# Optimization experiments

Measured on AMD Instinct MI355X. Metric: run time of the kernel, lower is better.

The kernel has to match this reference:

```python
import jax, jax.numpy as jnp
import numpy as np

TEMPERATURE = 0.07
NEG = -9e15  # matches torch masked_fill value
EPS = 1e-8   # torch.nn.functional.cosine_similarity eps


def setup_inputs() -> dict:
    key = jax.random.key(0)
    k1, k2 = jax.random.split(key)
    B, D = 4096, 512
    return {
        "feats1": jax.random.normal(k1, (B, D), dtype=jnp.float32),
        "feats2": jax.random.normal(k2, (B, D), dtype=jnp.float32),
    }


def reference(feats1, feats2):
    feats = jnp.concatenate([feats1, feats2], axis=0)            # [2N, D]
    n = feats.shape[0]
    # cosine similarity via normalize-once + GEMM (same math as the
    # broadcasted F.cosine_similarity, incl. per-vector eps clamp)
    norms = jnp.maximum(jnp.linalg.norm(feats, axis=-1, keepdims=True), EPS)
    fn = feats / norms                                            # [2N, D]
    cos_sim = fn @ fn.T                                           # [2N, 2N]
    # mask self-similarity BEFORE temperature division (as in torch code)
    idx = jnp.arange(n)
    cos_sim = jnp.where(idx[:, None] == idx[None, :], NEG, cos_sim)
    cos_sim = cos_sim / TEMPERATURE
    # positive pair: eye rolled by N rows -> column (i + N) mod 2N
    pos_idx = (idx + n // 2) % n
    pos = cos_sim[idx, pos_idx]                                   # [2N]
    nll = jnp.mean(-pos + jax.nn.logsumexp(cos_sim, axis=-1))
    # ranking: rank of the positive among [pos, masked negatives];
    # equals # of masked entries strictly greater than pos
    masked = jnp.where(idx[None, :] == pos_idx[:, None], NEG, cos_sim)
    rank = jnp.sum(masked > pos[:, None], axis=-1)                # int [2N]
    acc_top1 = jnp.mean((rank == 0).astype(jnp.float32))
    acc_top5 = jnp.mean((rank < 5).astype(jnp.float32))
    acc_mean_pos = 1.0 + jnp.mean(rank.astype(jnp.float32))
    return (nll, acc_top1, acc_top5, acc_mean_pos)
```

## Files before the change

kernel.cpp:

```cpp
#include <hip/hip_runtime.h>
#include <math.h>
#include <stdint.h>

#define NTOT   8192
#define HALF_N 4096
#define DIM    512
#define INV_T  14.2857142857142857f
#define NTILE  64
#define NBLK   2080

using s16x8 = __attribute__((ext_vector_type(8))) short;
using f32x4 = __attribute__((ext_vector_type(4))) float;

__device__ unsigned short g_fnb[NTOT * DIM];
__device__ float g_pos[NTOT];
__device__ float g_ps[NTILE * NTOT];
__device__ int   g_pc[NTILE * NTOT];
__device__ float g_sumexp[NTOT];
__device__ int   g_cnt[NTOT];

__device__ __forceinline__ float bf2f(unsigned short u) {
  union { unsigned int i; float f; } v; v.i = ((unsigned int)u) << 16; return v.f;
}
__device__ __forceinline__ unsigned short f2bf(float x) {
  union { float f; unsigned int i; } v; v.f = x;
  unsigned int u = v.i;
  return (unsigned short)((u + 0x7FFFu + ((u >> 16) & 1u)) >> 16);
}

__device__ __forceinline__ void gload16(const unsigned short* g, unsigned short* l) {
  __builtin_amdgcn_global_load_lds(
      (const __attribute__((address_space(1))) unsigned int*)g,
      (__attribute__((address_space(3))) unsigned int*)l, 16, 0, 0);
}

__global__ __launch_bounds__(256) void knorm(const float* __restrict__ f1,
                                             const float* __restrict__ f2) {
  const int tid  = threadIdx.x;
  const int wv   = tid >> 6;
  const int pi   = wv >> 1;
  const int half = wv & 1;
  const int lane = tid & 63;
  const int b    = blockIdx.x * 2 + pi;
  const int row  = b + half * HALF_N;

  const float* src = (half == 0) ? (f1 + (size_t)b * DIM) : (f2 + (size_t)b * DIM);
  float4 v0 = ((const float4*)src)[lane];
  float4 v1 = ((const float4*)src)[lane + 64];
  float ss = v0.x*v0.x + v0.y*v0.y + v0.z*v0.z + v0.w*v0.w
           + v1.x*v1.x + v1.y*v1.y + v1.z*v1.z + v1.w*v1.w;
  #pragma unroll
  for (int o = 32; o >= 1; o >>= 1) ss += __shfl_xor(ss, o, 64);
  const float sc = 1.0f / fmaxf(sqrtf(ss), 1e-8f);
  ushort4 h0, h1;
  h0.x = f2bf(v0.x * sc); h0.y = f2bf(v0.y * sc);
  h0.z = f2bf(v0.z * sc); h0.w = f2bf(v0.w * sc);
  h1.x = f2bf(v1.x * sc); h1.y = f2bf(v1.y * sc);
  h1.z = f2bf(v1.z * sc); h1.w = f2bf(v1.w * sc);
  ushort4* dst = (ushort4*)(g_fnb + (size_t)row * DIM);
  dst[lane]      = h0;
  dst[lane + 64] = h1;

  __shared__ ushort4 sh[2][64][2];
  if (half == 1) { sh[pi][lane][0] = h0; sh[pi][lane][1] = h1; }
  __syncthreads();
  if (half == 0) {
    const ushort4 p0 = sh[pi][lane][0], p1 = sh[pi][lane][1];
    float s = bf2f(h0.x)*bf2f(p0.x) + bf2f(h0.y)*bf2f(p0.y)
            + bf2f(h0.z)*bf2f(p0.z) + bf2f(h0.w)*bf2f(p0.w)
            + bf2f(h1.x)*bf2f(p1.x) + bf2f(h1.y)*bf2f(p1.y)
            + bf2f(h1.z)*bf2f(p1.z) + bf2f(h1.w)*bf2f(p1.w);
    #pragma unroll
    for (int o = 32; o >= 1; o >>= 1) s += __shfl_xor(s, o, 64);
    if (lane == 0) { g_pos[b] = s; g_pos[b + HALF_N] = s; }
  }
}

__global__ __launch_bounds__(256, 4) void kmain() {
  __shared__ __align__(16) unsigned short As[128 * 64];
  __shared__ __align__(16) unsigned short Bs[128 * 64];
  __shared__ float sRowS[128]; __shared__ int sRowC[128];
  __shared__ float sColS[128]; __shared__ int sColC[128];

  int t = (blockIdx.x & 7) * (NBLK / 8) + (blockIdx.x >> 3);
  int bi = 0, rem = NTILE;
  while (t >= rem) { t -= rem; --rem; ++bi; }
  const int bj = bi + t;
  const bool offdiag = (bi != bj);
  const int i0 = bi * 128, j0 = bj * 128;

  const int tid  = threadIdx.x;
  const int lane = tid & 63;
  const int w    = tid >> 6;
  const int wr   = (w >> 1) * 64;
  const int wc   = (w & 1) * 64;
  const int lrow = lane & 15;
  const int lq   = lane >> 4;

  const int rsub = lane >> 3;
  const int lcb  = (lane & 7) ^ rsub;
  const unsigned short* Ag = g_fnb + (size_t)(i0 + w * 32 + rsub) * DIM + lcb * 8;
  const unsigned short* Bg = g_fnb + (size_t)(j0 + w * 32 + rsub) * DIM + lcb * 8;
  unsigned short* Al = &As[w * 32 * 64];
  unsigned short* Bl = &Bs[w * 32 * 64];

  f32x4 acc[4][4];
  #pragma unroll
  for (int a = 0; a < 4; ++a)
    #pragma unroll
    for (int bb = 0; bb < 4; ++bb) { acc[a][bb][0]=0.f; acc[a][bb][1]=0.f; acc[a][bb][2]=0.f; acc[a][bb][3]=0.f; }

  const unsigned short* Bls = offdiag ? (const unsigned short*)Bs
                                      : (const unsigned short*)As;

  for (int kt = 0; kt < 8; ++kt) {
    __syncthreads();
    const int kb = kt * 64;
    #pragma unroll
    for (int q = 0; q < 4; ++q) {
      gload16(Ag + (size_t)(q * 8) * DIM + kb, Al + q * 512);
      if (offdiag) gload16(Bg + (size_t)(q * 8) * DIM + kb, Bl + q * 512);
    }
    __syncthreads();

    #pragma unroll
    for (int kk = 0; kk < 2; ++kk) {
      s16x8 af[4], bf[4];
      #pragma unroll
      for (int mi = 0; mi < 4; ++mi) {
        const int r = wr + mi * 16 + lrow;
        af[mi] = *(const s16x8*)(&As[r * 64 + (((kk * 4 + lq) ^ (lrow & 7)) * 8)]);
      }
      #pragma unroll
      for (int ni = 0; ni < 4; ++ni) {
        const int r = wc + ni * 16 + lrow;
        bf[ni] = *(const s16x8*)(&Bls[r * 64 + (((kk * 4 + lq) ^ (lrow & 7)) * 8)]);
      }
      #pragma unroll
      for (int mi = 0; mi < 4; ++mi)
        #pragma unroll
        for (int ni = 0; ni < 4; ++ni)
          acc[mi][ni] = __builtin_amdgcn_mfma_f32_16x16x32_bf16(af[mi], bf[ni], acc[mi][ni], 0, 0, 0);
    }
  }

  if (tid < 128) { sRowS[tid] = 0.f; sRowC[tid] = 0; sColS[tid] = 0.f; sColC[tid] = 0; }
  __syncthreads();

  #pragma unroll
  for (int mi = 0; mi < 4; ++mi) {
    #pragma unroll
    for (int r = 0; r < 4; ++r) {
      const int ridx = wr + mi * 16 + lq * 4 + r;
      const int i  = i0 + ridx;
      const float pv = g_pos[i];
      float s = 0.f; int c = 0;
      #pragma unroll
      for (int ni = 0; ni < 4; ++ni) {
        const int j = j0 + wc + ni * 16 + lrow;
        const float v = acc[mi][ni][r];
        const float e = __expf(v * INV_T);
        const bool diag = (j == i);
        s += diag ? 0.f : e;
        c += (!diag && (j != (i ^ HALF_N)) && (v > pv)) ? 1 : 0;
      }
      #pragma unroll
      for (int o = 1; o < 16; o <<= 1) {
        s += __shfl_xor(s, o, 64);
        c += __shfl_xor(c, o, 64);
      }
      if (lrow == 0) {
        atomicAdd(&sRowS[ridx], s);
        atomicAdd(&sRowC[ridx], c);
      }
    }
  }

  if (offdiag) {
    #pragma unroll
    for (int ni = 0; ni < 4; ++ni) {
      const int cidx = wc + ni * 16 + lrow;
      const int j  = j0 + cidx;
      const float pj = g_pos[j];
      float s = 0.f; int c = 0;
      #pragma unroll
      for (int mi = 0; mi < 4; ++mi) {
        #pragma unroll
        for (int r = 0; r < 4; ++r) {
          const int i = i0 + wr + mi * 16 + lq * 4 + r;
          const float v = acc[mi][ni][r];
          s += __expf(v * INV_T);
          c += ((i != (j ^ HALF_N)) && (v > pj)) ? 1 : 0;
        }
      }
      s += __shfl_xor(s, 16, 64); s += __shfl_xor(s, 32, 64);
      c += __shfl_xor(c, 16, 64); c += __shfl_xor(c, 32, 64);
      if (lq == 0) {
        atomicAdd(&sColS[cidx], s);
        atomicAdd(&sColC[cidx], c);
      }
    }
  }
  __syncthreads();

  if (tid < 128) {
    g_ps[(size_t)bj * NTOT + i0 + tid] = sRowS[tid];
    g_pc[(size_t)bj * NTOT + i0 + tid] = sRowC[tid];
  } else if (offdiag && tid < 256) {
    const int r2 = tid - 128;
    g_ps[(size_t)bi * NTOT + j0 + r2] = sColS[r2];
    g_pc[(size_t)bi * NTOT + j0 + r2] = sColC[r2];
  }
}

__global__ __launch_bounds__(256) void kred() {
  const int i = blockIdx.x * 256 + threadIdx.x;
  float s = 0.f; int c = 0;
  #pragma unroll 8
  for (int sl = 0; sl < NTILE; ++sl) {
    s += g_ps[(size_t)sl * NTOT + i];
    c += g_pc[(size_t)sl * NTOT + i];
  }
  g_sumexp[i] = s;
  g_cnt[i] = c;
}

__global__ __launch_bounds__(1024) void kfin(float* __restrict__ out) {
  const int tid = threadIdx.x;
  float nll = 0.f, t1 = 0.f, t5 = 0.f, mr = 0.f;
  for (int i = tid; i < NTOT; i += 1024) {
    nll += -g_pos[i] * INV_T + logf(g_sumexp[i]);
    const int c = g_cnt[i];
    t1 += (c == 0) ? 1.f : 0.f;
    t5 += (c < 5) ? 1.f : 0.f;
    mr += (float)c;
  }
  #pragma unroll
  for (int o = 32; o >= 1; o >>= 1) {
    nll += __shfl_xor(nll, o, 64);
    t1  += __shfl_xor(t1, o, 64);
    t5  += __shfl_xor(t5, o, 64);
    mr  += __shfl_xor(mr, o, 64);
  }
  __shared__ float red[16][4];
  const int wv = tid >> 6, lane = tid & 63;
  if (lane == 0) { red[wv][0] = nll; red[wv][1] = t1; red[wv][2] = t5; red[wv][3] = mr; }
  __syncthreads();
  if (tid == 0) {
    float a = 0.f, b = 0.f, c = 0.f, d = 0.f;
    for (int k = 0; k < 16; ++k) { a += red[k][0]; b += red[k][1]; c += red[k][2]; d += red[k][3]; }
    out[0] = a / (float)NTOT;
    out[1] = b / (float)NTOT;
    out[2] = c / (float)NTOT;
    out[3] = 1.f + d / (float)NTOT;
  }
}

extern "C" void kernel_launch(void* const* d_in, const int* in_sizes, int n_in,
                              void* d_out, int out_size, void* d_ws, size_t ws_size,
                              hipStream_t stream) {
  const float* f1 = (const float*)d_in[0];
  const float* f2 = (const float*)d_in[1];
  float* out = (float*)d_out;

  knorm<<<dim3(2048), dim3(256), 0, stream>>>(f1, f2);
  kmain<<<dim3(NBLK), dim3(256), 0, stream>>>();
  kred <<<dim3(32),   dim3(256), 0, stream>>>();
  kfin <<<dim3(1),    dim3(1024), 0, stream>>>(out);
}
```

Baseline: 157.4 us.

## Fuse reduction and finalize kernels, reuse LDS, supertile scheduling, raise occupancy

Merges the per-row partial reduction and the final scalar reduction into one kernel. A last-block atomic ticket finalizes the outputs, which removes one launch. In the main GEMM kernel, the row and column stat buffers are aliased onto the A tile LDS, with an added barrier, so LDS per block shrinks. The launch bound is raised from 4 to 5 blocks per SIMD/CU. Triangular tiles are remapped into 16x16 supertile groups to improve L2 locality of B tiles. The changes risk register spilling under the tighter bound and add an extra sync.

```diff
diff --git a/kernel.cpp b/kernel.cpp
--- a/kernel.cpp
+++ b/kernel.cpp
@@ -14,10 +14,14 @@
 
 __device__ unsigned short g_fnb[NTOT * DIM];
 __device__ float g_pos[NTOT];
-__device__ float g_ps[NTILE * NTOT];
-__device__ int   g_pc[NTILE * NTOT];
-__device__ float g_sumexp[NTOT];
-__device__ int   g_cnt[NTOT];
+__device__ float g_ps[(size_t)NTILE * NTOT];
+__device__ int   g_pc[(size_t)NTILE * NTOT];
+__device__ float g_part4[32 * 4];
+__device__ int   g_tick2;
+
+__constant__ int c_pre[11] = {0,136,392,648,904,1040,1296,1552,1688,1944,2080};
+__constant__ int c_gi[10]  = {0,0,0,0,1,1,1,2,2,3};
+__constant__ int c_gj[10]  = {0,1,2,3,1,2,3,2,3,3};
 
 __device__ __forceinline__ float bf2f(unsigned short u) {
   union { unsigned int i; float f; } v; v.i = ((unsigned int)u) << 16; return v.f;
@@ -43,6 +47,9 @@
   const int lane = tid & 63;
   const int b    = blockIdx.x * 2 + pi;
   const int row  = b + half * HALF_N;
+
+  if (blockIdx.x == 0 && tid == 0)
+    __hip_atomic_store(&g_tick2, 0, __ATOMIC_RELAXED, __HIP_MEMORY_SCOPE_AGENT);
 
   const float* src = (half == 0) ? (f1 + (size_t)b * DIM) : (f2 + (size_t)b * DIM);
   float4 v0 = ((const float4*)src)[lane];
@@ -76,16 +83,28 @@
   }
 }
 
-__global__ __launch_bounds__(256, 4) void kmain() {
+__global__ __launch_bounds__(256, 5) void kmain() {
   __shared__ __align__(16) unsigned short As[128 * 64];
   __shared__ __align__(16) unsigned short Bs[128 * 64];
-  __shared__ float sRowS[128]; __shared__ int sRowC[128];
-  __shared__ float sColS[128]; __shared__ int sColC[128];
-
-  int t = (blockIdx.x & 7) * (NBLK / 8) + (blockIdx.x >> 3);
-  int bi = 0, rem = NTILE;
-  while (t >= rem) { t -= rem; --rem; ++bi; }
-  const int bj = bi + t;
+  float* sRowS = reinterpret_cast<float*>(As);
+  int*   sRowC = reinterpret_cast<int*>(sRowS + 128);
+  float* sColS = reinterpret_cast<float*>(sRowC + 128);
+  int*   sColC = reinterpret_cast<int*>(sColS + 128);
+
+  const int t_sw = (blockIdx.x & 7) * (NBLK / 8) + (blockIdx.x >> 3);
+  int sp = 0;
+  while (t_sw >= c_pre[sp + 1]) ++sp;
+  int l = t_sw - c_pre[sp];
+  int lbi, lbj;
+  if (c_gi[sp] == c_gj[sp]) {
+    int r16 = 16; lbi = 0;
+    while (l >= r16) { l -= r16; --r16; ++lbi; }
+    lbj = lbi + l;
+  } else {
+    lbi = l >> 4; lbj = l & 15;
+  }
+  const int bi = c_gi[sp] * 16 + lbi;
+  const int bj = c_gj[sp] * 16 + lbj;
   const bool offdiag = (bi != bj);
   const int i0 = bi * 128, j0 = bj * 128;
 
@@ -144,6 +163,7 @@
     }
   }
 
+  __syncthreads();
   if (tid < 128) { sRowS[tid] = 0.f; sRowC[tid] = 0; sColS[tid] = 0.f; sColC[tid] = 0; }
   __syncthreads();
 
@@ -213,28 +233,19 @@
   }
 }
 
-__global__ __launch_bounds__(256) void kred() {
-  const int i = blockIdx.x * 256 + threadIdx.x;
+__global__ __launch_bounds__(256) void kredfin(float* __restrict__ out) {
+  const int tid = threadIdx.x;
+  const int i = blockIdx.x * 256 + tid;
   float s = 0.f; int c = 0;
   #pragma unroll 8
   for (int sl = 0; sl < NTILE; ++sl) {
     s += g_ps[(size_t)sl * NTOT + i];
     c += g_pc[(size_t)sl * NTOT + i];
   }
-  g_sumexp[i] = s;
-  g_cnt[i] = c;
-}
-
-__global__ __launch_bounds__(1024) void kfin(float* __restrict__ out) {
-  const int tid = threadIdx.x;
-  float nll = 0.f, t1 = 0.f, t5 = 0.f, mr = 0.f;
-  for (int i = tid; i < NTOT; i += 1024) {
-    nll += -g_pos[i] * INV_T + logf(g_sumexp[i]);
-    const int c = g_cnt[i];
-    t1 += (c == 0) ? 1.f : 0.f;
-    t5 += (c < 5) ? 1.f : 0.f;
-    mr += (float)c;
-  }
+  float nll = -g_pos[i] * INV_T + logf(s);
+  float t1 = (c == 0) ? 1.f : 0.f;
+  float t5 = (c < 5) ? 1.f : 0.f;
+  float mr = (float)c;
   #pragma unroll
   for (int o = 32; o >= 1; o >>= 1) {
     nll += __shfl_xor(nll, o, 64);
@@ -242,17 +253,35 @@
     t5  += __shfl_xor(t5, o, 64);
     mr  += __shfl_xor(mr, o, 64);
   }
-  __shared__ float red[16][4];
+  __shared__ float red[4][4];
   const int wv = tid >> 6, lane = tid & 63;
   if (lane == 0) { red[wv][0] = nll; red[wv][1] = t1; red[wv][2] = t5; red[wv][3] = mr; }
   __syncthreads();
   if (tid == 0) {
-    float a = 0.f, b = 0.f, c = 0.f, d = 0.f;
-    for (int k = 0; k < 16; ++k) { a += red[k][0]; b += red[k][1]; c += red[k][2]; d += red[k][3]; }
-    out[0] = a / (float)NTOT;
-    out[1] = b / (float)NTOT;
-    out[2] = c / (float)NTOT;
-    out[3] = 1.f + d / (float)NTOT;
+    float a = 0.f, b = 0.f, cc = 0.f, d = 0.f;
+    #pragma unroll
+    for (int k = 0; k < 4; ++k) { a += red[k][0]; b += red[k][1]; cc += red[k][2]; d += red[k][3]; }
+    g_part4[blockIdx.x * 4 + 0] = a;
+    g_part4[blockIdx.x * 4 + 1] = b;
+    g_part4[blockIdx.x * 4 + 2] = cc;
+    g_part4[blockIdx.x * 4 + 3] = d;
+    __builtin_amdgcn_fence(__ATOMIC_RELEASE, "agent");
+    const int old = __hip_atomic_fetch_add(&g_tick2, 1,
+                        __ATOMIC_RELAXED, __HIP_MEMORY_SCOPE_AGENT);
+    if (old == 31) {
+      __builtin_amdgcn_fence(__ATOMIC_ACQUIRE, "agent");
+      float A = 0.f, B = 0.f, C = 0.f, D = 0.f;
+      for (int k = 0; k < 32; ++k) {
+        A += g_part4[k * 4 + 0];
+        B += g_part4[k * 4 + 1];
+        C += g_part4[k * 4 + 2];
+        D += g_part4[k * 4 + 3];
+      }
+      out[0] = A / (float)NTOT;
+      out[1] = B / (float)NTOT;
+      out[2] = C / (float)NTOT;
+      out[3] = 1.f + D / (float)NTOT;
+    }
   }
 }
 
@@ -263,8 +292,7 @@
   const float* f2 = (const float*)d_in[1];
   float* out = (float*)d_out;
 
-  knorm<<<dim3(2048), dim3(256), 0, stream>>>(f1, f2);
-  kmain<<<dim3(NBLK), dim3(256), 0, stream>>>();
-  kred <<<dim3(32),   dim3(256), 0, stream>>>();
-  kfin <<<dim3(1),    dim3(1024), 0, stream>>>(out);
-}
+  knorm  <<<dim3(2048), dim3(256), 0, stream>>>(f1, f2);
+  kmain  <<<dim3(NBLK), dim3(256), 0, stream>>>();
+  kredfin<<<dim3(32),   dim3(256), 0, stream>>>(out);
+}
```

Measured after the change: 327.5 us. 2.08x slower.
